# Optimization experiments

Hardware: AMD Instinct MI355X
Metric: run time of the kernel (lower is better)

The kernel has to match this reference:

```python
import jax, jax.numpy as jnp
import numpy as np
import math

R, S, HC, MAX_L = 4, 6, 64, 100
NH = R + 2 * S  # 16 heads
D = NH * HC     # 1024


def _signed_pow(base, L):
    # base: [h,1,1] (possibly negative), L: [t,t] integer-valued float
    mag = jnp.exp(L * jnp.log(jnp.abs(base)))
    sgn = jnp.where(base < 0, 1.0 - 2.0 * (L % 2), 1.0)
    return mag * sgn


def setup_inputs() -> dict:
    key = jax.random.key(0)
    ks = jax.random.split(key, 12)
    b, t = 4, 2048
    x = jax.random.normal(ks[0], (b, t, D), dtype=jnp.float32)
    mu = jax.random.uniform(ks[1], (1,), minval=-3.0, maxval=3.0)
    flag = jnp.where(jax.random.randint(ks[2], (R,), 0, 2) == 0, -1.0, 1.0)
    lam = (jax.random.uniform(ks[3], (R,), minval=0.6, maxval=0.98) * flag)[:, None, None]
    gamma_c1 = jnp.tanh(jax.random.uniform(ks[4], (S,)) + 1.0)[:, None, None]
    gamma_c2 = jnp.tanh(jax.random.uniform(ks[5], (S,)) + 1.0)[:, None, None]
    theta_c1 = jnp.full((S, 1, 1), math.pi / 4, dtype=jnp.float32)
    theta_c2 = jnp.full((S, 1, 1), math.pi / 4, dtype=jnp.float32)
    sc = 1.0 / np.sqrt(D)
    Wq = jax.random.normal(ks[6], (D, D), dtype=jnp.float32) * sc
    Wk = jax.random.normal(ks[7], (D, D), dtype=jnp.float32) * sc
    Wv = jax.random.normal(ks[8], (D, D), dtype=jnp.float32) * sc
    Wf = jax.random.normal(ks[9], (D, D), dtype=jnp.float32) * sc
    bq = jnp.zeros((D,)); bk = jnp.zeros((D,)); bv = jnp.zeros((D,)); bf = jnp.zeros((D,))
    return dict(x=x, mu=mu, lam=lam, gamma_c1=gamma_c1, gamma_c2=gamma_c2,
                theta_c1=theta_c1, theta_c2=theta_c2,
                Wq=Wq, bq=bq, Wk=Wk, bk=bk, Wv=Wv, bv=bv, Wf=Wf, bf=bf)


def _positional(t, lam, gamma_c1, gamma_c2, theta_c1, theta_c2, dtype):
    # L[i,j] = min(max(i-j,0), MAX_L); strictly-lower-triangular mask
    mask = jnp.tril(jnp.ones((t, t), dtype=dtype), -1)
    L = jnp.minimum(jnp.cumsum(mask, axis=0), float(MAX_L))
    P_R = _signed_pow(lam, L) * mask                                   # [r,t,t]
    P_C1 = _signed_pow(gamma_c1, L) * mask * jnp.sin(theta_c1 * L)     # [s,t,t]
    P_C2 = _signed_pow(gamma_c2, L) * mask * jnp.cos(theta_c2 * L)     # [s,t,t]
    return jnp.concatenate([P_R, P_C1, P_C2], axis=0)                  # [H,t,t]


def reference(x, mu, lam, gamma_c1, gamma_c2, theta_c1, theta_c2,
              Wq, bq, Wk, bk, Wv, bv, Wf, bf):
    b, t, d = x.shape
    P = _positional(t, lam, gamma_c1, gamma_c2, theta_c1, theta_c2, x.dtype)
    Q = (x @ Wq.T + bq).reshape(b, t, NH, HC)
    K = (x @ Wk.T + bk).reshape(b, t, NH, HC)
    V = (x @ Wv.T + bv).reshape(b, t, NH, HC)
    scores = jnp.einsum('bqhd,bkhd->bhqk', Q, K)  # no 1/sqrt(d) scaling (faithful)
    att = jax.nn.softmax(scores, axis=-1)
    w = jax.nn.sigmoid(mu)[0]
    blend = (1.0 - w) * att + w * P[None]         # [b,H,t,t]
    out = jnp.einsum('bhqk,bkhd->bqhd', blend, V).reshape(b, t, NH * HC)
    return out @ Wf.T + bf
```

## Files before the change

kernel.cpp:

```cpp
#include <hip/hip_runtime.h>
#include <math.h>
#include <stdint.h>
#include <stddef.h>

typedef _Float16 f16;
typedef _Float16 f16x8 __attribute__((ext_vector_type(8)));
typedef _Float16 f16x4 __attribute__((ext_vector_type(4)));
typedef __fp16 fp16x2 __attribute__((ext_vector_type(2)));
typedef float f32x4 __attribute__((ext_vector_type(4)));
typedef float f32x16 __attribute__((ext_vector_type(16)));
typedef float fvec4 __attribute__((ext_vector_type(4)));
typedef unsigned int u32x4 __attribute__((ext_vector_type(4)));
typedef int i32x2 __attribute__((ext_vector_type(2)));

#define MFMA16F16(a, b, c) __builtin_amdgcn_mfma_f32_16x16x32_f16((a), (b), (c), 0, 0, 0)
#define MFMA32F16(a, b, c) __builtin_amdgcn_mfma_f32_32x32x16_f16((a), (b), (c), 0, 0, 0)

static constexpr int kT = 2048;
static constexpr int kB = 4;
static constexpr int kD = 1024;
static constexpr int kNH = 16;
static constexpr int kM = kB * kT;
static constexpr int kMAXL = 100;
static constexpr float kLOG2E = 1.4426950408889634f;

static constexpr size_t SZ_XH = (size_t)kM * kD * 2;
static constexpr size_t SZ_W = (size_t)kD * kD * 2;
static constexpr size_t OFF_TAB = 0;
static constexpr size_t OFF_XH = 8192;
static constexpr size_t OFF_WQ = OFF_XH + SZ_XH;
static constexpr size_t OFF_WK = OFF_WQ + SZ_W;
static constexpr size_t OFF_WV = OFF_WK + SZ_W;
static constexpr size_t OFF_WF = OFF_WV + SZ_W;
static constexpr size_t OFF_Q = OFF_WF + SZ_W;
static constexpr size_t OFF_K = OFF_Q + SZ_XH;
static constexpr size_t OFF_V = OFF_K + SZ_XH;
static constexpr size_t OFF_P = OFF_V + SZ_XH;
static constexpr size_t WS_NEED = OFF_P + SZ_XH;

__device__ __forceinline__ unsigned int pk_f16(float a, float b) {
  fp16x2 h = __builtin_amdgcn_cvt_pkrtz(a, b);
  return __builtin_bit_cast(unsigned int, h);
}

__device__ __forceinline__ i32x2 pl32swap(unsigned a, unsigned b) {
  return __builtin_amdgcn_permlane32_swap((int)a, (int)b, false, false);
}

__global__ void mk_tab_kernel(const float* __restrict__ mu, const float* __restrict__ lam,
                              const float* __restrict__ g1, const float* __restrict__ g2,
                              const float* __restrict__ th1, const float* __restrict__ th2,
                              float* __restrict__ tab) {
  const float w = 1.0f / (1.0f + expf(-mu[0]));
  for (int e = threadIdx.x; e < kNH * (kMAXL + 1); e += blockDim.x) {
    const int h = e / (kMAXL + 1);
    const int L = e - h * (kMAXL + 1);
    const float Lf = (float)L;
    float v;
    if (h < 4) {
      const float base = lam[h];
      const float mag = expf(Lf * logf(fabsf(base)));
      const float sgn = (base < 0.0f && (L & 1)) ? -1.0f : 1.0f;
      v = mag * sgn;
    } else if (h < 10) {
      const int s = h - 4;
      v = expf(Lf * logf(g1[s])) * sinf(th1[s] * Lf);
    } else {
      const int s = h - 10;
      v = expf(Lf * logf(g2[s])) * cosf(th2[s] * Lf);
    }
    tab[e] = w * v;
  }
  if (threadIdx.x == 0) tab[kNH * (kMAXL + 1)] = 1.0f - w;
}

__global__ void cvt_kernel(const float* __restrict__ s, f16* __restrict__ d, int n4) {
  int i = blockIdx.x * blockDim.x + threadIdx.x;
  const int stride = gridDim.x * blockDim.x;
  for (; i < n4; i += stride) {
    fvec4 v = ((const fvec4*)s)[i];
    f16x4 o;
    o[0] = (f16)v[0]; o[1] = (f16)v[1]; o[2] = (f16)v[2]; o[3] = (f16)v[3];
    ((f16x4*)d)[i] = o;
  }
}

template <typename OutT, bool BIAS_ROW>
__global__ __launch_bounds__(256, 3) void gemm_bt_kernel(
    const f16* __restrict__ A, const f16* __restrict__ B, const float* __restrict__ bias,
    OutT* __restrict__ C, int M, int N, int K, float oscale) {
  __shared__ f16 As[128][32];
  __shared__ f16 Bs[128][32];
  const int tid = threadIdx.x;
  const int lane = tid & 63;
  const int wave = tid >> 6;
  const int quad = lane >> 4;
  const int l16 = lane & 15;
  const int nb = N >> 7;
  const int bm = blockIdx.x / nb;
  const int bn = blockIdx.x - bm * nb;
  const int m0 = bm << 7;
  const int n0 = bn << 7;
  const int wm = (wave & 1) << 6;
  const int wn = (wave >> 1) << 6;

  const int srow = tid >> 2;
  const int scol = (tid & 3) << 3;
  const f16* Ap = A + (size_t)(m0 + srow) * K + scol;
  const f16* Bp = B + (size_t)(n0 + srow) * K + scol;
  const size_t rstep = (size_t)64 * K;

  f32x4 acc[4][4];
#pragma unroll
  for (int i = 0; i < 4; i++)
#pragma unroll
    for (int j = 0; j < 4; j++) acc[i][j] = (f32x4){0.f, 0.f, 0.f, 0.f};

  f16x8 ra0 = *(const f16x8*)(Ap);
  f16x8 ra1 = *(const f16x8*)(Ap + rstep);
  f16x8 rb0 = *(const f16x8*)(Bp);
  f16x8 rb1 = *(const f16x8*)(Bp + rstep);

  for (int k0 = 0; k0 < K; k0 += 32) {
    __syncthreads();
    *(f16x8*)&As[srow][scol] = ra0;
    *(f16x8*)&As[srow + 64][scol] = ra1;
    *(f16x8*)&Bs[srow][scol] = rb0;
    *(f16x8*)&Bs[srow + 64][scol] = rb1;
    __syncthreads();
    if (k0 + 32 < K) {
      ra0 = *(const f16x8*)(Ap + (k0 + 32));
      ra1 = *(const f16x8*)(Ap + rstep + (k0 + 32));
      rb0 = *(const f16x8*)(Bp + (k0 + 32));
      rb1 = *(const f16x8*)(Bp + rstep + (k0 + 32));
    }
    f16x8 af[4], bf[4];
#pragma unroll
    for (int i = 0; i < 4; i++) af[i] = *(const f16x8*)&As[wm + i * 16 + l16][quad * 8];
#pragma unroll
    for (int i = 0; i < 4; i++) bf[i] = *(const f16x8*)&Bs[wn + i * 16 + l16][quad * 8];
#pragma unroll
    for (int mi = 0; mi < 4; mi++)
#pragma unroll
      for (int ni = 0; ni < 4; ni++) acc[mi][ni] = MFMA16F16(af[mi], bf[ni], acc[mi][ni]);
  }

#pragma unroll
  for (int mi = 0; mi < 4; mi++) {
    const int rbase = m0 + wm + mi * 16 + quad * 4;
#pragma unroll
    for (int ni = 0; ni < 4; ni++) {
      const int gc = n0 + wn + ni * 16 + l16;
      const float bcol = BIAS_ROW ? 0.0f : bias[gc];
#pragma unroll
      for (int r = 0; r < 4; r++) {
        const int gr = rbase + r;
        float v = acc[mi][ni][r] + (BIAS_ROW ? bias[gr] : bcol);
        v *= oscale;
        C[(size_t)gr * N + gc] = (OutT)v;
      }
    }
  }
}

__global__ __launch_bounds__(256, 4) void qkv_kernel(
    const f16* __restrict__ xh, const f16* __restrict__ wq, const f16* __restrict__ wk,
    const f16* __restrict__ wv, const float* __restrict__ bq, const float* __restrict__ bk,
    const float* __restrict__ bv, f16* __restrict__ Qp, f16* __restrict__ Kp,
    f16* __restrict__ Vt) {
  __shared__ f16 As[128][32];
  __shared__ f16 Bs[128][32];
  const int g = blockIdx.x >> 9;
  const int inner = blockIdx.x & 511;
  const f16* A = (g == 2) ? wv : xh;
  const f16* B = (g == 0) ? wq : ((g == 1) ? wk : xh);
  const float* bias = (g == 0) ? bq : ((g == 1) ? bk : bv);
  f16* C = (g == 0) ? Qp : ((g == 1) ? Kp : Vt);
  const int N = (g == 2) ? kM : kD;
  const int K = kD;
  const float oscale = (g == 0) ? kLOG2E : 1.0f;
  const bool bias_row = (g == 2);
  const int nbs = (g == 2) ? 6 : 3;

  const int tid = threadIdx.x;
  const int lane = tid & 63;
  const int wave = tid >> 6;
  const int quad = lane >> 4;
  const int l16 = lane & 15;
  const int bm = inner >> nbs;
  const int bn = inner & ((1 << nbs) - 1);
  const int m0 = bm << 7;
  const int n0 = bn << 7;
  const int wm = (wave & 1) << 6;
  const int wn = (wave >> 1) << 6;

  const int srow = tid >> 2;
  const int scol = (tid & 3) << 3;
  const f16* Ap = A + (size_t)(m0 + srow) * K + scol;
  const f16* Bp = B + (size_t)(n0 + srow) * K + scol;
  const size_t rstep = (size_t)64 * K;

  f32x4 acc[4][4];
#pragma unroll
  for (int i = 0; i < 4; i++)
#pragma unroll
    for (int j = 0; j < 4; j++) acc[i][j] = (f32x4){0.f, 0.f, 0.f, 0.f};

  f16x8 ra0 = *(const f16x8*)(Ap);
  f16x8 ra1 = *(const f16x8*)(Ap + rstep);
  f16x8 rb0 = *(const f16x8*)(Bp);
  f16x8 rb1 = *(const f16x8*)(Bp + rstep);

  for (int k0 = 0; k0 < K; k0 += 32) {
    __syncthreads();
    *(f16x8*)&As[srow][scol] = ra0;
    *(f16x8*)&As[srow + 64][scol] = ra1;
    *(f16x8*)&Bs[srow][scol] = rb0;
    *(f16x8*)&Bs[srow + 64][scol] = rb1;
    __syncthreads();
    if (k0 + 32 < K) {
      ra0 = *(const f16x8*)(Ap + (k0 + 32));
      ra1 = *(const f16x8*)(Ap + rstep + (k0 + 32));
      rb0 = *(const f16x8*)(Bp + (k0 + 32));
      rb1 = *(const f16x8*)(Bp + rstep + (k0 + 32));
    }
    f16x8 af[4], bf[4];
#pragma unroll
    for (int i = 0; i < 4; i++) af[i] = *(const f16x8*)&As[wm + i * 16 + l16][quad * 8];
#pragma unroll
    for (int i = 0; i < 4; i++) bf[i] = *(const f16x8*)&Bs[wn + i * 16 + l16][quad * 8];
#pragma unroll
    for (int mi = 0; mi < 4; mi++)
#pragma unroll
      for (int ni = 0; ni < 4; ni++) acc[mi][ni] = MFMA16F16(af[mi], bf[ni], acc[mi][ni]);
  }

#pragma unroll
  for (int mi = 0; mi < 4; mi++) {
    const int rbase = m0 + wm + mi * 16 + quad * 4;
#pragma unroll
    for (int ni = 0; ni < 4; ni++) {
      const int gc = n0 + wn + ni * 16 + l16;
      const float bcol = bias_row ? 0.0f : bias[gc];
#pragma unroll
      for (int r = 0; r < 4; r++) {
        const int gr = rbase + r;
        float v = acc[mi][ni][r] + (bias_row ? bias[gr] : bcol);
        v *= oscale;
        C[(size_t)gr * N + gc] = (f16)v;
      }
    }
  }
}

__global__ __launch_bounds__(256, 3) void attn_kernel(
    const f16* __restrict__ Qh, const f16* __restrict__ Kh, const f16* __restrict__ Vt,
    const float* __restrict__ tabg, f16* __restrict__ Pb) {
  __shared__ f16 Ks[128][68];
  __shared__ f16 Vs[64][132];
  __shared__ float tab_s[101];

  const int tid = threadIdx.x;
  const int lane = tid & 63;
  const int wave = tid >> 6;
  const int l31 = lane & 31;
  const int hi = lane >> 5;
  const int hi8 = hi * 8;
  const int xcd = blockIdx.x & 7;
  const int rest = blockIdx.x >> 3;
  const int qt = rest & 15;
  const int combo = (rest >> 4) * 8 + xcd;
  const int h = combo & 15;
  const int bi = combo >> 4;

  if (tid < 101) tab_s[tid] = tabg[h * 101 + tid];
  const float one_m_w = tabg[kNH * 101];
  const float tab100f = tabg[h * 101 + kMAXL];

  const int qblk = qt * 128;
  const int qw0 = qblk + wave * 32;
  const int qg = qw0 + l31;
  const size_t bt0 = (size_t)bi * kT;

  f16x8 qf[4];
#pragma unroll
  for (int kc = 0; kc < 4; kc++)
    qf[kc] = *(const f16x8*)(Qh + (bt0 + qg) * kD + h * 64 + kc * 16 + hi8);

  f32x16 Oat[2], Opc[2];
  f32x16 Lacc;
#pragma unroll
  for (int dt = 0; dt < 2; dt++)
#pragma unroll
    for (int r = 0; r < 16; r++) {
      Oat[dt][r] = 0.f;
      Opc[dt][r] = 0.f;
    }
#pragma unroll
  for (int r = 0; r < 16; r++) Lacc[r] = 0.f;
  float mrow = -INFINITY;

  const int sr8 = tid >> 3, sp8 = tid & 7;
  const int sr16 = tid >> 4, sp16 = tid & 15;

  f16x8 cf, ones;
  {
    const f16 cth = (f16)tab100f;
#pragma unroll
    for (int ii = 0; ii < 8; ii++) {
      cf[ii] = cth;
      ones[ii] = (f16)1.0f;
    }
  }

  for (int j0 = 0; j0 < kT; j0 += 128) {
    __syncthreads();
#pragma unroll
    for (int u = 0; u < 4; u++) {
      const int jr = sr8 + u * 32;
      *(f16x8*)&Ks[jr][sp8 * 8] = *(const f16x8*)(Kh + (bt0 + j0 + jr) * kD + h * 64 + sp8 * 8);
    }
#pragma unroll
    for (int u = 0; u < 4; u++) {
      const int d = sr16 + u * 16;
      *(f16x8*)&Vs[d][sp16 * 8] =
          *(const f16x8*)(Vt + (size_t)(h * 64 + d) * kM + bt0 + j0 + sp16 * 8);
    }
    __syncthreads();

#pragma unroll
    for (int c = 0; c < 2; c++) {
      f32x16 s[2];
#pragma unroll
      for (int jt = 0; jt < 2; jt++)
#pragma unroll
        for (int r = 0; r < 16; r++) s[jt][r] = 0.f;
#pragma unroll
      for (int kc = 0; kc < 4; kc++) {
        f16x8 ka = *(const f16x8*)&Ks[c * 64 + l31][kc * 16 + hi8];
        f16x8 kb = *(const f16x8*)&Ks[c * 64 + 32 + l31][kc * 16 + hi8];
        s[0] = MFMA32F16(ka, qf[kc], s[0]);
        s[1] = MFMA32F16(kb, qf[kc], s[1]);
      }

      float mx = s[0][0];
#pragma unroll
      for (int jt = 0; jt < 2; jt++)
#pragma unroll
        for (int r = 0; r < 16; r++) mx = fmaxf(mx, s[jt][r]);
      mx = fmaxf(mx, __shfl_xor(mx, 32));
      if (!__all(mx <= mrow + 8.0f)) {
        const float mnew = fmaxf(mrow, mx);
        const float al = __builtin_amdgcn_exp2f(mrow - mnew);
        mrow = mnew;
#pragma unroll
        for (int dt = 0; dt < 2; dt++)
#pragma unroll
          for (int r = 0; r < 16; r++) Oat[dt][r] *= al;
        Lacc[0] *= al;
      }

#pragma unroll
      for (int jt = 0; jt < 2; jt++) {
        unsigned w[8];
#pragma unroll
        for (int k = 0; k < 8; k++) {
          const float e0 = __builtin_amdgcn_exp2f(s[jt][2 * k] - mrow);
          const float e1 = __builtin_amdgcn_exp2f(s[jt][2 * k + 1] - mrow);
          w[k] = pk_f16(e0, e1);
        }
        i32x2 a0 = pl32swap(w[0], w[2]);
        i32x2 a1 = pl32swap(w[1], w[3]);
        i32x2 b0 = pl32swap(w[4], w[6]);
        i32x2 b1 = pl32swap(w[5], w[7]);
        u32x4 ue = {(unsigned)a0.x, (unsigned)a1.x, (unsigned)a0.y, (unsigned)a1.y};
        u32x4 uo = {(unsigned)b0.x, (unsigned)b1.x, (unsigned)b0.y, (unsigned)b1.y};
        const f16x8 fe = __builtin_bit_cast(f16x8, ue);
        const f16x8 fo = __builtin_bit_cast(f16x8, uo);
#pragma unroll
        for (int dt = 0; dt < 2; dt++) {
          f16x8 ve = *(const f16x8*)&Vs[dt * 32 + l31][c * 64 + jt * 32 + hi8];
          Oat[dt] = MFMA32F16(ve, fe, Oat[dt]);
        }
        Lacc = MFMA32F16(ones, fe, Lacc);
#pragma unroll
        for (int dt = 0; dt < 2; dt++) {
          f16x8 vo = *(const f16x8*)&Vs[dt * 32 + l31][c * 64 + jt * 32 + 16 + hi8];
          Oat[dt] = MFMA32F16(vo, fo, Oat[dt]);
        }
        Lacc = MFMA32F16(ones, fo, Lacc);
      }
    }

    if (j0 + 228 <= qw0) {
#pragma unroll
      for (int jc = 0; jc < 8; jc++)
#pragma unroll
        for (int dt = 0; dt < 2; dt++) {
          f16x8 vf = *(const f16x8*)&Vs[dt * 32 + l31][jc * 16 + hi8];
          Opc[dt] = MFMA32F16(vf, cf, Opc[dt]);
        }
    }
  }

  {
    const float inv = one_m_w / Lacc[0];
#pragma unroll
    for (int dt = 0; dt < 2; dt++)
#pragma unroll
      for (int r = 0; r < 16; r++) Oat[dt][r] = Oat[dt][r] * inv + Opc[dt][r];
  }

#pragma unroll
  for (int tb = 0; tb < 2; tb++) {
    const int jb = qblk - 128 + tb * 128;
    if (jb >= 0) {
      __syncthreads();
#pragma unroll
      for (int u = 0; u < 4; u++) {
        const int d = sr16 + u * 16;
        *(f16x8*)&Vs[d][sp16 * 8] =
            *(const f16x8*)(Vt + (size_t)(h * 64 + d) * kM + bt0 + jb + sp16 * 8);
      }
      __syncthreads();
#pragma unroll
      for (int jc = 0; jc < 8; jc++) {
        f16x8 wf;
#pragma unroll
        for (int e = 0; e < 8; e++) {
          const int j = jb + jc * 16 + hi8 + e;
          const int dlt = qg - j;
          float pv = 0.0f;
          if (dlt > 0) pv = tab_s[dlt > kMAXL ? kMAXL : dlt];
          wf[e] = (f16)pv;
        }
#pragma unroll
        for (int dt = 0; dt < 2; dt++) {
          f16x8 vf = *(const f16x8*)&Vs[dt * 32 + l31][jc * 16 + hi8];
          Oat[dt] = MFMA32F16(vf, wf, Oat[dt]);
        }
      }
    }
  }

  {
    f16* sw = &Ks[wave * 32][0];
#pragma unroll
    for (int dt = 0; dt < 2; dt++)
#pragma unroll
      for (int r = 0; r < 16; r++) {
        const int d = dt * 32 + (r & 3) + 8 * (r >> 2) + 4 * hi;
        sw[l31 * 68 + d] = (f16)Oat[dt][r];
      }
#pragma unroll
    for (int u = 0; u < 4; u++) {
      const int qr = lane >> 1;
      const int c0 = (lane & 1) * 32 + u * 8;
      f16x8 ofr = *(const f16x8*)&sw[qr * 68 + c0];
      *(f16x8*)(Pb + (bt0 + qw0 + qr) * kD + h * 64 + c0) = ofr;
    }
  }
}

extern "C" void kernel_launch(void* const* d_in, const int* in_sizes, int n_in, void* d_out,
                              int out_size, void* d_ws, size_t ws_size, hipStream_t stream) {
  const float* x = (const float*)d_in[0];
  const float* mu = (const float*)d_in[1];
  const float* lam = (const float*)d_in[2];
  const float* g1 = (const float*)d_in[3];
  const float* g2 = (const float*)d_in[4];
  const float* th1 = (const float*)d_in[5];
  const float* th2 = (const float*)d_in[6];
  const float* Wq = (const float*)d_in[7];
  const float* bq = (const float*)d_in[8];
  const float* Wk = (const float*)d_in[9];
  const float* bk = (const float*)d_in[10];
  const float* Wv = (const float*)d_in[11];
  const float* bv = (const float*)d_in[12];
  const float* Wf = (const float*)d_in[13];
  const float* bf = (const float*)d_in[14];

  if (ws_size < WS_NEED) return;

  char* ws = (char*)d_ws;
  float* tab = (float*)(ws + OFF_TAB);
  f16* xh = (f16*)(ws + OFF_XH);
  f16* wqh = (f16*)(ws + OFF_WQ);
  f16* wkh = (f16*)(ws + OFF_WK);
  f16* wvh = (f16*)(ws + OFF_WV);
  f16* wfh = (f16*)(ws + OFF_WF);
  f16* Qp = (f16*)(ws + OFF_Q);
  f16* Kp = (f16*)(ws + OFF_K);
  f16* Vtp = (f16*)(ws + OFF_V);
  f16* Pbp = (f16*)(ws + OFF_P);

  mk_tab_kernel<<<1, 256, 0, stream>>>(mu, lam, g1, g2, th1, th2, tab);
  cvt_kernel<<<2048, 256, 0, stream>>>(x, xh, kM * kD / 4);
  cvt_kernel<<<1024, 256, 0, stream>>>(Wq, wqh, kD * kD / 4);
  cvt_kernel<<<1024, 256, 0, stream>>>(Wk, wkh, kD * kD / 4);
  cvt_kernel<<<1024, 256, 0, stream>>>(Wv, wvh, kD * kD / 4);
  cvt_kernel<<<1024, 256, 0, stream>>>(Wf, wfh, kD * kD / 4);

  qkv_kernel<<<1536, 256, 0, stream>>>(xh, wqh, wkh, wvh, bq, bk, bv, Qp, Kp, Vtp);

  attn_kernel<<<1024, 256, 0, stream>>>(Qp, Kp, Vtp, tab, Pbp);

  gemm_bt_kernel<float, false><<<512, 256, 0, stream>>>(Pbp, wfh, bf, (float*)d_out, kM, kD, kD,
                                                        1.0f);
}
```

Baseline: 368.9 us.

## Fuse positional tail into main attention loop and batch QK over full tile

Computes all four 32-key score tiles per 128-key block before the softmax, using a single tree-reduced row max and one rescale check per block instead of one per 64-key half. The near-diagonal positional contribution is now accumulated into Opc inside the main loop, while those V tiles are already resident in shared memory. This removes the separate tail pass that reloaded V tiles with extra barriers. The qkv kernel's launch-bounds occupancy hint drops from 4 to 3, trading occupancy for registers; the larger live score set in attention raises register pressure.

```diff
diff --git a/kernel.cpp b/kernel.cpp
--- a/kernel.cpp
+++ b/kernel.cpp
@@ -163,7 +163,7 @@
   }
 }
 
-__global__ __launch_bounds__(256, 4) void qkv_kernel(
+__global__ __launch_bounds__(256, 3) void qkv_kernel(
     const f16* __restrict__ xh, const f16* __restrict__ wq, const f16* __restrict__ wk,
     const f16* __restrict__ wv, const float* __restrict__ bq, const float* __restrict__ bk,
     const float* __restrict__ bv, f16* __restrict__ Qp, f16* __restrict__ Kp,
@@ -328,26 +328,33 @@
     }
     __syncthreads();
 
-#pragma unroll
-    for (int c = 0; c < 2; c++) {
-      f32x16 s[2];
-#pragma unroll
-      for (int jt = 0; jt < 2; jt++)
-#pragma unroll
-        for (int r = 0; r < 16; r++) s[jt][r] = 0.f;
-#pragma unroll
-      for (int kc = 0; kc < 4; kc++) {
-        f16x8 ka = *(const f16x8*)&Ks[c * 64 + l31][kc * 16 + hi8];
-        f16x8 kb = *(const f16x8*)&Ks[c * 64 + 32 + l31][kc * 16 + hi8];
-        s[0] = MFMA32F16(ka, qf[kc], s[0]);
-        s[1] = MFMA32F16(kb, qf[kc], s[1]);
-      }
-
-      float mx = s[0][0];
-#pragma unroll
-      for (int jt = 0; jt < 2; jt++)
-#pragma unroll
-        for (int r = 0; r < 16; r++) mx = fmaxf(mx, s[jt][r]);
+    f32x16 s[4];
+#pragma unroll
+    for (int cj = 0; cj < 4; cj++)
+#pragma unroll
+      for (int r = 0; r < 16; r++) s[cj][r] = 0.f;
+#pragma unroll
+    for (int kc = 0; kc < 4; kc++) {
+      const f16x8 qk = qf[kc];
+#pragma unroll
+      for (int cj = 0; cj < 4; cj++) {
+        f16x8 kf = *(const f16x8*)&Ks[cj * 32 + l31][kc * 16 + hi8];
+        s[cj] = MFMA32F16(kf, qk, s[cj]);
+      }
+    }
+
+    {
+      float t8[8];
+#pragma unroll
+      for (int k = 0; k < 8; k++) {
+        const int cj = k >> 1, b = (k & 1) * 8;
+        const float a0 = fmaxf(fmaxf(s[cj][b], s[cj][b + 1]), fmaxf(s[cj][b + 2], s[cj][b + 3]));
+        const float a1 =
+            fmaxf(fmaxf(s[cj][b + 4], s[cj][b + 5]), fmaxf(s[cj][b + 6], s[cj][b + 7]));
+        t8[k] = fmaxf(a0, a1);
+      }
+      float mx = fmaxf(fmaxf(fmaxf(t8[0], t8[1]), fmaxf(t8[2], t8[3])),
+                       fmaxf(fmaxf(t8[4], t8[5]), fmaxf(t8[6], t8[7])));
       mx = fmaxf(mx, __shfl_xor(mx, 32));
       if (!__all(mx <= mrow + 8.0f)) {
         const float mnew = fmaxf(mrow, mx);
@@ -359,37 +366,37 @@
           for (int r = 0; r < 16; r++) Oat[dt][r] *= al;
         Lacc[0] *= al;
       }
-
-#pragma unroll
-      for (int jt = 0; jt < 2; jt++) {
-        unsigned w[8];
-#pragma unroll
-        for (int k = 0; k < 8; k++) {
-          const float e0 = __builtin_amdgcn_exp2f(s[jt][2 * k] - mrow);
-          const float e1 = __builtin_amdgcn_exp2f(s[jt][2 * k + 1] - mrow);
-          w[k] = pk_f16(e0, e1);
-        }
-        i32x2 a0 = pl32swap(w[0], w[2]);
-        i32x2 a1 = pl32swap(w[1], w[3]);
-        i32x2 b0 = pl32swap(w[4], w[6]);
-        i32x2 b1 = pl32swap(w[5], w[7]);
-        u32x4 ue = {(unsigned)a0.x, (unsigned)a1.x, (unsigned)a0.y, (unsigned)a1.y};
-        u32x4 uo = {(unsigned)b0.x, (unsigned)b1.x, (unsigned)b0.y, (unsigned)b1.y};
-        const f16x8 fe = __builtin_bit_cast(f16x8, ue);
-        const f16x8 fo = __builtin_bit_cast(f16x8, uo);
-#pragma unroll
-        for (int dt = 0; dt < 2; dt++) {
-          f16x8 ve = *(const f16x8*)&Vs[dt * 32 + l31][c * 64 + jt * 32 + hi8];
-          Oat[dt] = MFMA32F16(ve, fe, Oat[dt]);
-        }
-        Lacc = MFMA32F16(ones, fe, Lacc);
-#pragma unroll
-        for (int dt = 0; dt < 2; dt++) {
-          f16x8 vo = *(const f16x8*)&Vs[dt * 32 + l31][c * 64 + jt * 32 + 16 + hi8];
-          Oat[dt] = MFMA32F16(vo, fo, Oat[dt]);
-        }
-        Lacc = MFMA32F16(ones, fo, Lacc);
-      }
+    }
+
+#pragma unroll
+    for (int cj = 0; cj < 4; cj++) {
+      unsigned w[8];
+#pragma unroll
+      for (int k = 0; k < 8; k++) {
+        const float e0 = __builtin_amdgcn_exp2f(s[cj][2 * k] - mrow);
+        const float e1 = __builtin_amdgcn_exp2f(s[cj][2 * k + 1] - mrow);
+        w[k] = pk_f16(e0, e1);
+      }
+      i32x2 a0 = pl32swap(w[0], w[2]);
+      i32x2 a1 = pl32swap(w[1], w[3]);
+      i32x2 b0 = pl32swap(w[4], w[6]);
+      i32x2 b1 = pl32swap(w[5], w[7]);
+      u32x4 ue = {(unsigned)a0.x, (unsigned)a1.x, (unsigned)a0.y, (unsigned)a1.y};
+      u32x4 uo = {(unsigned)b0.x, (unsigned)b1.x, (unsigned)b0.y, (unsigned)b1.y};
+      const f16x8 fe = __builtin_bit_cast(f16x8, ue);
+      const f16x8 fo = __builtin_bit_cast(f16x8, uo);
+#pragma unroll
+      for (int dt = 0; dt < 2; dt++) {
+        f16x8 ve = *(const f16x8*)&Vs[dt * 32 + l31][cj * 32 + hi8];
+        Oat[dt] = MFMA32F16(ve, fe, Oat[dt]);
+      }
+      Lacc = MFMA32F16(ones, fe, Lacc);
+#pragma unroll
+      for (int dt = 0; dt < 2; dt++) {
+        f16x8 vo = *(const f16x8*)&Vs[dt * 32 + l31][cj * 32 + 16 + hi8];
+        Oat[dt] = MFMA32F16(vo, fo, Oat[dt]);
+      }
+      Lacc = MFMA32F16(ones, fo, Lacc);
     }
 
     if (j0 + 228 <= qw0) {
@@ -401,34 +408,14 @@
           Opc[dt] = MFMA32F16(vf, cf, Opc[dt]);
         }
     }
-  }
-
-  {
-    const float inv = one_m_w / Lacc[0];
-#pragma unroll
-    for (int dt = 0; dt < 2; dt++)
-#pragma unroll
-      for (int r = 0; r < 16; r++) Oat[dt][r] = Oat[dt][r] * inv + Opc[dt][r];
-  }
-
-#pragma unroll
-  for (int tb = 0; tb < 2; tb++) {
-    const int jb = qblk - 128 + tb * 128;
-    if (jb >= 0) {
-      __syncthreads();
-#pragma unroll
-      for (int u = 0; u < 4; u++) {
-        const int d = sr16 + u * 16;
-        *(f16x8*)&Vs[d][sp16 * 8] =
-            *(const f16x8*)(Vt + (size_t)(h * 64 + d) * kM + bt0 + jb + sp16 * 8);
-      }
-      __syncthreads();
+
+    if (j0 == qblk - 128 || j0 == qblk) {
 #pragma unroll
       for (int jc = 0; jc < 8; jc++) {
         f16x8 wf;
 #pragma unroll
         for (int e = 0; e < 8; e++) {
-          const int j = jb + jc * 16 + hi8 + e;
+          const int j = j0 + jc * 16 + hi8 + e;
           const int dlt = qg - j;
           float pv = 0.0f;
           if (dlt > 0) pv = tab_s[dlt > kMAXL ? kMAXL : dlt];
@@ -437,12 +424,21 @@
 #pragma unroll
         for (int dt = 0; dt < 2; dt++) {
           f16x8 vf = *(const f16x8*)&Vs[dt * 32 + l31][jc * 16 + hi8];
-          Oat[dt] = MFMA32F16(vf, wf, Oat[dt]);
+          Opc[dt] = MFMA32F16(vf, wf, Opc[dt]);
         }
       }
     }
   }
 
+  {
+    const float inv = one_m_w / Lacc[0];
+#pragma unroll
+    for (int dt = 0; dt < 2; dt++)
+#pragma unroll
+      for (int r = 0; r < 16; r++) Oat[dt][r] = Oat[dt][r] * inv + Opc[dt][r];
+  }
+
+  __syncthreads();
   {
     f16* sw = &Ks[wave * 32][0];
 #pragma unroll
```

Result: slower. 420.6 us (+14.0%).
